# Optimization experiments

Measured on AMD Instinct MI355X. Metric: run time of the kernel, lower is better.

The kernel has to match this reference:

```python
import jax, jax.numpy as jnp
import numpy as np

B, S, H, T, F, L = 32, 512, 1024, 100, 512, 5  # batch, seq, hidden, num_topics, topic_hidden, n_langs
EPS = 1e-5


def _layernorm(x, g, b):
    mu = jnp.mean(x, axis=-1, keepdims=True)
    var = jnp.mean((x - mu) ** 2, axis=-1, keepdims=True)
    return (x - mu) * jax.lax.rsqrt(var + EPS) * g + b


def setup_inputs() -> dict:
    key = jax.random.key(0)
    ks = jax.random.split(key, 16)
    sc = 0.02
    return {
        "sequence_output": jax.random.normal(ks[0], (B, S, H), dtype=jnp.float32),
        "attention_mask": jnp.ones((B, S), dtype=jnp.float32),
        "language_ids": jax.random.randint(ks[1], (B,), 0, L, dtype=jnp.int32),
        "lda_features": jax.random.uniform(ks[2], (B, T), dtype=jnp.float32),
        # per-language adapter params (stacked over L)
        "W1": jax.random.normal(ks[3], (L, H, H), dtype=jnp.float32) * sc,
        "b1": jnp.zeros((L, H), dtype=jnp.float32),
        "g1": jnp.ones((L, H), dtype=jnp.float32),
        "beta1": jnp.zeros((L, H), dtype=jnp.float32),
        "W2": jax.random.normal(ks[4], (L, H, H), dtype=jnp.float32) * sc,
        "b2": jnp.zeros((L, H), dtype=jnp.float32),
        # topic fusion params
        "Wf": jax.random.normal(ks[5], (H + T, F), dtype=jnp.float32) * sc,
        "bf": jnp.zeros((F,), dtype=jnp.float32),
        "gf": jnp.ones((F,), dtype=jnp.float32),
        "betaf": jnp.zeros((F,), dtype=jnp.float32),
    }


def reference(sequence_output, attention_mask, language_ids, lda_features,
              W1, b1, g1, beta1, W2, b2, Wf, bf, gf, betaf):
    # Apply every language adapter to the full batch, then mask-accumulate
    # (faithful to the original anti-pattern).
    adapted = jnp.zeros_like(sequence_output)
    for lang in range(L):
        h = jnp.einsum("bsh,he->bse", sequence_output, W1[lang]) + b1[lang]
        h = jax.nn.relu(_layernorm(h, g1[lang], beta1[lang]))
        h = jnp.einsum("bsh,he->bse", h, W2[lang]) + b2[lang]
        lang_mask = (language_ids == lang).astype(sequence_output.dtype)[:, None, None]
        adapted = adapted + lang_mask * h
    # masked mean pool over sequence
    masked = adapted * attention_mask[:, :, None]
    pooled = masked.sum(axis=1) / attention_mask.sum(axis=1)[:, None]  # [B, H]
    combined = jnp.concatenate([pooled, lda_features], axis=-1)        # [B, H+T]
    fused = _layernorm(combined @ Wf + bf, gf, betaf)
    return jax.nn.relu(fused)  # dropout is identity in eval
```

## Files before the change

### kernel.cpp

```cpp
#include <hip/hip_runtime.h>
#include <hip/hip_bf16.h>
#include <stdint.h>

#define Bq 32
#define Sq 512
#define Hq 1024
#define Tq 100
#define Fq 512
#define Lq 5
#define EPSq 1e-5f

typedef float fx4 __attribute__((ext_vector_type(4)));
typedef __bf16 bfx8 __attribute__((ext_vector_type(8)));
typedef unsigned short u16x8 __attribute__((ext_vector_type(8)));

static __device__ __forceinline__ unsigned short f2bf(float f) {
  unsigned int u = __builtin_bit_cast(unsigned int, f);
  return (unsigned short)((u + 0x7fffu + ((u >> 16) & 1u)) >> 16);
}
static __device__ __forceinline__ float bf2f(unsigned short s) {
  return __builtin_bit_cast(float, ((unsigned int)s) << 16);
}
static __device__ __forceinline__ void gl_lds16(const void* g, void* l) {
  __builtin_amdgcn_global_load_lds(
      (const __attribute__((address_space(1))) unsigned int*)(uintptr_t)g,
      (__attribute__((address_space(3))) unsigned int*)(uintptr_t)l,
      16, 0, 0);
}

__global__ void k_prep(const float* __restrict__ seq, unsigned short* __restrict__ seqbf,
                       const float* __restrict__ w1, unsigned short* __restrict__ w1t) {
  int blk = blockIdx.x;
  int tid = threadIdx.x;
  if (blk < 8192) {
    int i = blk * 256 + tid;
    const float4* p = (const float4*)seq + (size_t)i * 2;
    float4 a = p[0], b = p[1];
    u16x8 o;
    o[0] = f2bf(a.x); o[1] = f2bf(a.y); o[2] = f2bf(a.z); o[3] = f2bf(a.w);
    o[4] = f2bf(b.x); o[5] = f2bf(b.y); o[6] = f2bf(b.z); o[7] = f2bf(b.w);
    *((u16x8*)seqbf + i) = o;
  } else {
    __shared__ float t[32][33];
    int bb = blk - 8192;
    int l = bb >> 10; int rem = bb & 1023; int tr = rem >> 5; int tc = rem & 31;
    const float* src = w1 + (size_t)l * Hq * Hq;
    unsigned short* dst = w1t + (size_t)l * Hq * Hq;
    int tx = tid & 31, ty = tid >> 5;
#pragma unroll
    for (int p = 0; p < 4; p++)
      t[ty + 8 * p][tx] = src[(size_t)(tr * 32 + ty + 8 * p) * Hq + tc * 32 + tx];
    __syncthreads();
#pragma unroll
    for (int p = 0; p < 4; p++)
      dst[(size_t)(tc * 32 + ty + 8 * p) * Hq + tr * 32 + tx] = f2bf(t[tx][ty + 8 * p]);
  }
}

__global__ __launch_bounds__(512, 2) void k_gemm1(const unsigned short* __restrict__ seqbf,
                                                  const unsigned short* __restrict__ w1t,
                                                  const float* __restrict__ b1,
                                                  const int* __restrict__ lid,
                                                  unsigned short* __restrict__ h1bf) {
  __shared__ short sA[4][256 * 32];
  __shared__ short sB[4][256 * 32];
  int bid = blockIdx.x;
  int g = bid & 63; int tn = bid >> 6;
  int b = g >> 1; int tm = g & 1;
  int lang = lid[b];
  const unsigned short* Ab = seqbf + (size_t)b * Sq * Hq + (size_t)tm * 256 * Hq;
  const unsigned short* Bb = w1t + (size_t)lang * Hq * Hq + (size_t)tn * 256 * Hq;

  int tid = threadIdx.x;
  int lane = tid & 63; int wid = tid >> 6;
  int wr = wid >> 2, wc = wid & 3;
  int fr = lane & 15;
  int q = lane >> 4;
  int key = ((fr >> 1) & 7) << 4;

  const unsigned short* gA[2]; const unsigned short* gB[2]; int dstOff[2];
#pragma unroll
  for (int j = 0; j < 2; j++) {
    int p = (tid + j * 512) * 16;
    int l = p ^ ((p >> 3) & 0x70);
    int R = l >> 6, qa = (l >> 4) & 3;
    gA[j] = Ab + (size_t)R * Hq + qa * 8;
    gB[j] = Bb + (size_t)R * Hq + qa * 8;
    dstOff[j] = p;
  }

  int aOff[8], bOff[4];
#pragma unroll
  for (int m = 0; m < 8; m++)
    aOff[m] = ((wr * 128 + m * 16 + fr) * 64 + q * 16) ^ key;
#pragma unroll
  for (int n = 0; n < 4; n++)
    bOff[n] = ((wc * 64 + n * 16 + fr) * 64 + q * 16) ^ key;

  fx4 acc[8][4];
#pragma unroll
  for (int m = 0; m < 8; m++)
#pragma unroll
    for (int n = 0; n < 4; n++) acc[m][n] = (fx4){0.f, 0.f, 0.f, 0.f};

#pragma unroll
  for (int s = 0; s < 3; s++) {
#pragma unroll
    for (int j = 0; j < 2; j++) {
      gl_lds16(gA[j] + s * 32, (char*)sA[s] + dstOff[j]);
      gl_lds16(gB[j] + s * 32, (char*)sB[s] + dstOff[j]);
    }
  }

  for (int hs = 0; hs < 32; hs++) {
    int cur = hs & 3;
    if (hs < 30)
      asm volatile("s_waitcnt vmcnt(8) lgkmcnt(0)\n\ts_barrier" ::: "memory");
    else if (hs == 30)
      asm volatile("s_waitcnt vmcnt(4) lgkmcnt(0)\n\ts_barrier" ::: "memory");
    else
      asm volatile("s_waitcnt vmcnt(0) lgkmcnt(0)\n\ts_barrier" ::: "memory");
    if (hs <= 28) {
      int slot = (hs + 3) & 3;
      int ko = (hs + 3) * 32;
#pragma unroll
      for (int j = 0; j < 2; j++) {
        gl_lds16(gA[j] + ko, (char*)sA[slot] + dstOff[j]);
        gl_lds16(gB[j] + ko, (char*)sB[slot] + dstOff[j]);
      }
    }
    const char* cA = (const char*)sA[cur];
    const char* cB = (const char*)sB[cur];
    bfx8 bf[4], af[8];
#pragma unroll
    for (int n = 0; n < 4; n++) bf[n] = *(const bfx8*)(cB + bOff[n]);
#pragma unroll
    for (int m = 0; m < 8; m++) af[m] = *(const bfx8*)(cA + aOff[m]);
    __builtin_amdgcn_s_setprio(1);
#pragma unroll
    for (int m = 0; m < 8; m++)
#pragma unroll
      for (int n = 0; n < 4; n++)
        acc[m][n] = __builtin_amdgcn_mfma_f32_16x16x32_bf16(af[m], bf[n], acc[m][n], 0, 0, 0);
    __builtin_amdgcn_s_setprio(0);
  }

  unsigned short* Cb = h1bf + (size_t)b * Sq * Hq;
  float bv[4];
#pragma unroll
  for (int n = 0; n < 4; n++)
    bv[n] = b1[lang * Hq + tn * 256 + wc * 64 + n * 16 + fr];
  int r0 = q * 4;
#pragma unroll
  for (int m = 0; m < 8; m++) {
#pragma unroll
    for (int n = 0; n < 4; n++) {
      int col = tn * 256 + wc * 64 + n * 16 + fr;
#pragma unroll
      for (int r = 0; r < 4; r++) {
        int row = tm * 256 + wr * 128 + m * 16 + r0 + r;
        Cb[(size_t)row * Hq + col] = f2bf(acc[m][n][r] + bv[n]);
      }
    }
  }
}

__global__ __launch_bounds__(256) void k_ln_pool(const unsigned short* __restrict__ h1bf,
                                                 const float* __restrict__ g1,
                                                 const float* __restrict__ be1,
                                                 const float* __restrict__ mask,
                                                 const int* __restrict__ lid,
                                                 float* __restrict__ partial) {
  __shared__ float sacc[4][1024];
  int blk = blockIdx.x; int b = blk >> 3; int ch = blk & 7;
  int tid = threadIdx.x; int lane = tid & 63; int w = tid >> 6;
  int lang = lid[b];
  int e0 = lane * 8;
  int e1 = 512 + lane * 8;

  const float4* gp = (const float4*)(g1 + (size_t)lang * Hq);
  const float4* bp = (const float4*)(be1 + (size_t)lang * Hq);
  float4 ga0 = gp[lane * 2], ga1 = gp[lane * 2 + 1];
  float4 gb0 = gp[128 + lane * 2], gb1 = gp[129 + lane * 2];
  float4 ba0 = bp[lane * 2], ba1 = bp[lane * 2 + 1];
  float4 bb0 = bp[128 + lane * 2], bb1 = bp[129 + lane * 2];
  float gA[8] = {ga0.x, ga0.y, ga0.z, ga0.w, ga1.x, ga1.y, ga1.z, ga1.w};
  float gB[8] = {gb0.x, gb0.y, gb0.z, gb0.w, gb1.x, gb1.y, gb1.z, gb1.w};
  float bA[8] = {ba0.x, ba0.y, ba0.z, ba0.w, ba1.x, ba1.y, ba1.z, ba1.w};
  float bB[8] = {bb0.x, bb0.y, bb0.z, bb0.w, bb1.x, bb1.y, bb1.z, bb1.w};

  float acc0[8] = {0, 0, 0, 0, 0, 0, 0, 0}, acc1[8] = {0, 0, 0, 0, 0, 0, 0, 0};

  for (int i = 0; i < 16; i++) {
    int s = ch * 64 + w * 16 + i;
    const unsigned short* rowp = h1bf + ((size_t)b * Sq + s) * Hq;
    u16x8 va = *(const u16x8*)(rowp + e0);
    u16x8 vb = *(const u16x8*)(rowp + e1);
    float xa[8], xb[8];
    float sum = 0.f, sq = 0.f;
#pragma unroll
    for (int j = 0; j < 8; j++) {
      xa[j] = bf2f(va[j]); sum += xa[j]; sq += xa[j] * xa[j];
      xb[j] = bf2f(vb[j]); sum += xb[j]; sq += xb[j] * xb[j];
    }
#pragma unroll
    for (int off = 1; off < 64; off <<= 1) {
      sum += __shfl_xor(sum, off, 64);
      sq += __shfl_xor(sq, off, 64);
    }
    float mu = sum * (1.f / Hq);
    float var = sq * (1.f / Hq) - mu * mu;
    float rstd = rsqrtf(var + EPSq);
    float mw = mask[b * Sq + s];
#pragma unroll
    for (int j = 0; j < 8; j++) {
      float y0 = fmaxf((xa[j] - mu) * rstd * gA[j] + bA[j], 0.f);
      float y1 = fmaxf((xb[j] - mu) * rstd * gB[j] + bB[j], 0.f);
      acc0[j] += mw * y0;
      acc1[j] += mw * y1;
    }
  }
#pragma unroll
  for (int j = 0; j < 8; j++) {
    sacc[w][e0 + j] = acc0[j];
    sacc[w][e1 + j] = acc1[j];
  }
  __syncthreads();
  int e = tid * 4;
#pragma unroll
  for (int j = 0; j < 4; j++)
    partial[(size_t)blk * Hq + e + j] =
        sacc[0][e + j] + sacc[1][e + j] + sacc[2][e + j] + sacc[3][e + j];
}

__global__ void k_reduce_pool(const float* __restrict__ partial, const float* __restrict__ mask,
                              float* __restrict__ pooled) {
  __shared__ float wsum[4];
  int b = blockIdx.x; int tid = threadIdx.x;
  float mv = mask[b * Sq + tid] + mask[b * Sq + 256 + tid];
#pragma unroll
  for (int off = 1; off < 64; off <<= 1) mv += __shfl_xor(mv, off, 64);
  if ((tid & 63) == 0) wsum[tid >> 6] = mv;
  __syncthreads();
  float inv = 1.0f / (wsum[0] + wsum[1] + wsum[2] + wsum[3]);
  int e = tid * 4;
#pragma unroll
  for (int j = 0; j < 4; j++) {
    float s = 0.f;
#pragma unroll
    for (int c = 0; c < 8; c++) s += partial[((size_t)b * 8 + c) * Hq + e + j];
    pooled[b * Hq + e + j] = s * inv;
  }
}

__global__ __launch_bounds__(256) void k_gemm2p(const float* __restrict__ pooled,
                                                const float* __restrict__ w2,
                                                const int* __restrict__ lid,
                                                float* __restrict__ g2part) {
  __shared__ float pl[256];
  int blk = blockIdx.x;
  int b = blk >> 3; int ch = (blk >> 2) & 1; int ks = blk & 3;
  int tid = threadIdx.x;
  int lang = lid[b];
  pl[tid] = pooled[b * Hq + ks * 256 + tid];
  __syncthreads();
  int col = ch * 512 + tid * 2;
  const float* W = w2 + (size_t)lang * Hq * Hq + (size_t)ks * 256 * Hq + col;
  float a0 = 0.f, a1 = 0.f;
  for (int e0 = 0; e0 < 256; e0 += 8) {
    float2 w[8];
#pragma unroll
    for (int j = 0; j < 8; j++) w[j] = *(const float2*)(W + (size_t)(e0 + j) * Hq);
#pragma unroll
    for (int j = 0; j < 8; j++) { float c = pl[e0 + j]; a0 += c * w[j].x; a1 += c * w[j].y; }
  }
  float2* dst = (float2*)(g2part + ((size_t)(b * 4 + ks) * Hq) + col);
  *dst = make_float2(a0, a1);
}

__global__ __launch_bounds__(256) void k_gemm2red(const float* __restrict__ g2part,
                                                  const float* __restrict__ b2,
                                                  const int* __restrict__ lid,
                                                  float* __restrict__ pooledf) {
  int b = blockIdx.x; int tid = threadIdx.x;
  int lang = lid[b];
  int col = tid * 4;
  float4 acc = *(const float4*)(b2 + (size_t)lang * Hq + col);
#pragma unroll
  for (int ks = 0; ks < 4; ks++) {
    float4 p = *(const float4*)(g2part + ((size_t)(b * 4 + ks) * Hq) + col);
    acc.x += p.x; acc.y += p.y; acc.z += p.z; acc.w += p.w;
  }
  *(float4*)(pooledf + (size_t)b * Hq + col) = acc;
}

__global__ __launch_bounds__(256) void k_fpart(const float* __restrict__ pooledf,
                                               const float* __restrict__ lda,
                                               const float* __restrict__ wf,
                                               float* __restrict__ fpart) {
  __shared__ float sc[128];
  int blk = blockIdx.x;
  int b = blk / 9, ks = blk % 9;
  int tid = threadIdx.x;
  int klen = (ks < 8) ? 128 : 100;
  int kbase = (ks < 8) ? ks * 128 : Hq;
  if (tid < klen) sc[tid] = (ks < 8) ? pooledf[b * Hq + kbase + tid] : lda[b * Tq + tid];
  __syncthreads();
  const float* W = wf + (size_t)kbase * Fq + tid * 2;
  float a0 = 0.f, a1 = 0.f;
  int k0 = 0;
  for (; k0 + 8 <= klen; k0 += 8) {
    float2 w[8];
#pragma unroll
    for (int j = 0; j < 8; j++) w[j] = *(const float2*)(W + (size_t)(k0 + j) * Fq);
#pragma unroll
    for (int j = 0; j < 8; j++) { float c = sc[k0 + j]; a0 += c * w[j].x; a1 += c * w[j].y; }
  }
  for (; k0 < klen; k0++) {
    float2 w = *(const float2*)(W + (size_t)k0 * Fq);
    float c = sc[k0];
    a0 += c * w.x; a1 += c * w.y;
  }
  float2* dst = (float2*)(fpart + (size_t)blk * Fq + tid * 2);
  *dst = make_float2(a0, a1);
}

__global__ __launch_bounds__(512) void k_final2(const float* __restrict__ fpart,
                                                const float* __restrict__ bff,
                                                const float* __restrict__ gf,
                                                const float* __restrict__ betaf,
                                                float* __restrict__ out) {
  __shared__ float rsum[8], rsq[8];
  int b = blockIdx.x; int tid = threadIdx.x;
  float acc = bff[tid];
#pragma unroll
  for (int ks = 0; ks < 9; ks++) acc += fpart[((size_t)b * 9 + ks) * Fq + tid];
  float s = acc, q = acc * acc;
#pragma unroll
  for (int off = 1; off < 64; off <<= 1) {
    s += __shfl_xor(s, off, 64);
    q += __shfl_xor(q, off, 64);
  }
  int w = tid >> 6, lane = tid & 63;
  if (lane == 0) { rsum[w] = s; rsq[w] = q; }
  __syncthreads();
  float S = 0.f, Q = 0.f;
#pragma unroll
  for (int i = 0; i < 8; i++) { S += rsum[i]; Q += rsq[i]; }
  float mu = S * (1.f / Fq);
  float var = Q * (1.f / Fq) - mu * mu;
  float y = (acc - mu) * rsqrtf(var + EPSq) * gf[tid] + betaf[tid];
  y = fmaxf(y, 0.f);
  out[b * Fq + tid] = y;
}

extern "C" void kernel_launch(void* const* d_in, const int* in_sizes, int n_in,
                              void* d_out, int out_size, void* d_ws, size_t ws_size,
                              hipStream_t stream) {
  const float* seq = (const float*)d_in[0];
  const float* mask = (const float*)d_in[1];
  const int* lid = (const int*)d_in[2];
  const float* lda = (const float*)d_in[3];
  const float* W1 = (const float*)d_in[4];
  const float* b1 = (const float*)d_in[5];
  const float* g1 = (const float*)d_in[6];
  const float* be1 = (const float*)d_in[7];
  const float* W2 = (const float*)d_in[8];
  const float* b2 = (const float*)d_in[9];
  const float* Wf = (const float*)d_in[10];
  const float* bff = (const float*)d_in[11];
  const float* gf = (const float*)d_in[12];
  const float* betaf = (const float*)d_in[13];
  float* out = (float*)d_out;

  char* ws = (char*)d_ws;
  unsigned short* seqbf = (unsigned short*)(ws);
  unsigned short* w1t = (unsigned short*)(ws + 33554432);
  unsigned short* h1bf = (unsigned short*)(ws + 44040192);
  float* partial = (float*)(ws + 77594624);
  float* pooled = (float*)(ws + 78643200);
  float* pooledf = (float*)(ws + 78774272);
  float* g2part = (float*)(ws + 78905344);
  float* fpart = (float*)(ws + 79429632);

  k_prep<<<13312, 256, 0, stream>>>(seq, seqbf, W1, w1t);
  k_gemm1<<<256, 512, 0, stream>>>(seqbf, w1t, b1, lid, h1bf);
  k_ln_pool<<<256, 256, 0, stream>>>(h1bf, g1, be1, mask, lid, partial);
  k_reduce_pool<<<32, 256, 0, stream>>>(partial, mask, pooled);
  k_gemm2p<<<256, 256, 0, stream>>>(pooled, W2, lid, g2part);
  k_gemm2red<<<32, 256, 0, stream>>>(g2part, b2, lid, pooledf);
  k_fpart<<<288, 256, 0, stream>>>(pooledf, lda, Wf, fpart);
  k_final2<<<32, 512, 0, stream>>>(fpart, bff, gf, betaf, out);
}
```

Measured before the change: 101.6 us.

## Fuse fp32-to-bf16 activation conversion into GEMM1 and merge small reduction kernels

Removes the separate sequence conversion pass: GEMM1 now loads fp32 activations into registers, converts to bf16 and writes swizzled LDS tiles, while B still uses direct global-to-LDS loads. The pooled reduction and bias-add reductions are folded into the downstream GEMV kernels, eliminating two launches and intermediate buffers. This trades a large extra memory pass for register pressure and VALU conversion work inside the GEMM main loop, with reworked wait counts.

```diff
diff --git a/kernel.cpp b/kernel.cpp
--- a/kernel.cpp
+++ b/kernel.cpp
@@ -21,6 +21,12 @@
 static __device__ __forceinline__ float bf2f(unsigned short s) {
   return __builtin_bit_cast(float, ((unsigned int)s) << 16);
 }
+static __device__ __forceinline__ u16x8 cvt8(float4 x0, float4 x1) {
+  u16x8 r;
+  r[0] = f2bf(x0.x); r[1] = f2bf(x0.y); r[2] = f2bf(x0.z); r[3] = f2bf(x0.w);
+  r[4] = f2bf(x1.x); r[5] = f2bf(x1.y); r[6] = f2bf(x1.z); r[7] = f2bf(x1.w);
+  return r;
+}
 static __device__ __forceinline__ void gl_lds16(const void* g, void* l) {
   __builtin_amdgcn_global_load_lds(
       (const __attribute__((address_space(1))) unsigned int*)(uintptr_t)g,
@@ -28,36 +34,24 @@
       16, 0, 0);
 }
 
-__global__ void k_prep(const float* __restrict__ seq, unsigned short* __restrict__ seqbf,
-                       const float* __restrict__ w1, unsigned short* __restrict__ w1t) {
+__global__ void k_prep(const float* __restrict__ w1, unsigned short* __restrict__ w1t) {
+  __shared__ float t[32][33];
   int blk = blockIdx.x;
+  int l = blk >> 10; int rem = blk & 1023; int tr = rem >> 5; int tc = rem & 31;
+  const float* src = w1 + (size_t)l * Hq * Hq;
+  unsigned short* dst = w1t + (size_t)l * Hq * Hq;
   int tid = threadIdx.x;
-  if (blk < 8192) {
-    int i = blk * 256 + tid;
-    const float4* p = (const float4*)seq + (size_t)i * 2;
-    float4 a = p[0], b = p[1];
-    u16x8 o;
-    o[0] = f2bf(a.x); o[1] = f2bf(a.y); o[2] = f2bf(a.z); o[3] = f2bf(a.w);
-    o[4] = f2bf(b.x); o[5] = f2bf(b.y); o[6] = f2bf(b.z); o[7] = f2bf(b.w);
-    *((u16x8*)seqbf + i) = o;
-  } else {
-    __shared__ float t[32][33];
-    int bb = blk - 8192;
-    int l = bb >> 10; int rem = bb & 1023; int tr = rem >> 5; int tc = rem & 31;
-    const float* src = w1 + (size_t)l * Hq * Hq;
-    unsigned short* dst = w1t + (size_t)l * Hq * Hq;
-    int tx = tid & 31, ty = tid >> 5;
-#pragma unroll
-    for (int p = 0; p < 4; p++)
-      t[ty + 8 * p][tx] = src[(size_t)(tr * 32 + ty + 8 * p) * Hq + tc * 32 + tx];
-    __syncthreads();
-#pragma unroll
-    for (int p = 0; p < 4; p++)
-      dst[(size_t)(tc * 32 + ty + 8 * p) * Hq + tr * 32 + tx] = f2bf(t[tx][ty + 8 * p]);
-  }
-}
-
-__global__ __launch_bounds__(512, 2) void k_gemm1(const unsigned short* __restrict__ seqbf,
+  int tx = tid & 31, ty = tid >> 5;
+#pragma unroll
+  for (int p = 0; p < 4; p++)
+    t[ty + 8 * p][tx] = src[(size_t)(tr * 32 + ty + 8 * p) * Hq + tc * 32 + tx];
+  __syncthreads();
+#pragma unroll
+  for (int p = 0; p < 4; p++)
+    dst[(size_t)(tc * 32 + ty + 8 * p) * Hq + tr * 32 + tx] = f2bf(t[tx][ty + 8 * p]);
+}
+
+__global__ __launch_bounds__(512, 2) void k_gemm1(const float* __restrict__ seq,
                                                   const unsigned short* __restrict__ w1t,
                                                   const float* __restrict__ b1,
                                                   const int* __restrict__ lid,
@@ -68,7 +62,7 @@
   int g = bid & 63; int tn = bid >> 6;
   int b = g >> 1; int tm = g & 1;
   int lang = lid[b];
-  const unsigned short* Ab = seqbf + (size_t)b * Sq * Hq + (size_t)tm * 256 * Hq;
+  const float* Abf = seq + (size_t)b * Sq * Hq + (size_t)tm * 256 * Hq;
   const unsigned short* Bb = w1t + (size_t)lang * Hq * Hq + (size_t)tn * 256 * Hq;
 
   int tid = threadIdx.x;
@@ -78,13 +72,21 @@
   int q = lane >> 4;
   int key = ((fr >> 1) & 7) << 4;
 
-  const unsigned short* gA[2]; const unsigned short* gB[2]; int dstOff[2];
+  const float* gAf0; const float* gAf1; int aW0, aW1;
+  {
+    int c0 = tid;        int R0 = c0 >> 2, q0 = c0 & 3; int y0 = R0 * 64 + q0 * 16;
+    int c1 = tid + 512;  int R1 = c1 >> 2, q1 = c1 & 3; int y1 = R1 * 64 + q1 * 16;
+    aW0 = y0 ^ ((y0 >> 3) & 0x70);
+    aW1 = y1 ^ ((y1 >> 3) & 0x70);
+    gAf0 = Abf + (size_t)R0 * Hq + q0 * 8;
+    gAf1 = Abf + (size_t)R1 * Hq + q1 * 8;
+  }
+  const unsigned short* gB[2]; int dstOff[2];
 #pragma unroll
   for (int j = 0; j < 2; j++) {
     int p = (tid + j * 512) * 16;
     int l = p ^ ((p >> 3) & 0x70);
     int R = l >> 6, qa = (l >> 4) & 3;
-    gA[j] = Ab + (size_t)R * Hq + qa * 8;
     gB[j] = Bb + (size_t)R * Hq + qa * 8;
     dstOff[j] = p;
   }
@@ -103,31 +105,43 @@
 #pragma unroll
     for (int n = 0; n < 4; n++) acc[m][n] = (fx4){0.f, 0.f, 0.f, 0.f};
 
+  float4 ra0a, ra0b, ra1a, ra1b;
+
+#pragma unroll
+  for (int t = 0; t < 2; t++) {
+    ra0a = *(const float4*)(gAf0 + t * 32); ra0b = *(const float4*)(gAf0 + t * 32 + 4);
+    ra1a = *(const float4*)(gAf1 + t * 32); ra1b = *(const float4*)(gAf1 + t * 32 + 4);
+    *(u16x8*)((char*)sA[t] + aW0) = cvt8(ra0a, ra0b);
+    *(u16x8*)((char*)sA[t] + aW1) = cvt8(ra1a, ra1b);
+  }
+  ra0a = *(const float4*)(gAf0 + 64); ra0b = *(const float4*)(gAf0 + 68);
+  ra1a = *(const float4*)(gAf1 + 64); ra1b = *(const float4*)(gAf1 + 68);
 #pragma unroll
   for (int s = 0; s < 3; s++) {
-#pragma unroll
-    for (int j = 0; j < 2; j++) {
-      gl_lds16(gA[j] + s * 32, (char*)sA[s] + dstOff[j]);
-      gl_lds16(gB[j] + s * 32, (char*)sB[s] + dstOff[j]);
-    }
+    gl_lds16(gB[0] + s * 32, (char*)sB[s] + dstOff[0]);
+    gl_lds16(gB[1] + s * 32, (char*)sB[s] + dstOff[1]);
   }
 
   for (int hs = 0; hs < 32; hs++) {
     int cur = hs & 3;
-    if (hs < 30)
-      asm volatile("s_waitcnt vmcnt(8) lgkmcnt(0)\n\ts_barrier" ::: "memory");
-    else if (hs == 30)
+    if (hs < 31)
       asm volatile("s_waitcnt vmcnt(4) lgkmcnt(0)\n\ts_barrier" ::: "memory");
     else
       asm volatile("s_waitcnt vmcnt(0) lgkmcnt(0)\n\ts_barrier" ::: "memory");
+    if (hs <= 29) {
+      int sa = (hs + 2) & 3;
+      *(u16x8*)((char*)sA[sa] + aW0) = cvt8(ra0a, ra0b);
+      *(u16x8*)((char*)sA[sa] + aW1) = cvt8(ra1a, ra1b);
+    }
     if (hs <= 28) {
-      int slot = (hs + 3) & 3;
       int ko = (hs + 3) * 32;
-#pragma unroll
-      for (int j = 0; j < 2; j++) {
-        gl_lds16(gA[j] + ko, (char*)sA[slot] + dstOff[j]);
-        gl_lds16(gB[j] + ko, (char*)sB[slot] + dstOff[j]);
-      }
+      ra0a = *(const float4*)(gAf0 + ko); ra0b = *(const float4*)(gAf0 + ko + 4);
+      ra1a = *(const float4*)(gAf1 + ko); ra1b = *(const float4*)(gAf1 + ko + 4);
+    }
+    if (hs <= 28) {
+      int ko = (hs + 3) * 32;
+      gl_lds16(gB[0] + ko, (char*)sB[(hs + 3) & 3] + dstOff[0]);
+      gl_lds16(gB[1] + ko, (char*)sB[(hs + 3) & 3] + dstOff[1]);
     }
     const char* cA = (const char*)sA[cur];
     const char* cB = (const char*)sB[cur];
@@ -233,36 +247,27 @@
         sacc[0][e + j] + sacc[1][e + j] + sacc[2][e + j] + sacc[3][e + j];
 }
 
-__global__ void k_reduce_pool(const float* __restrict__ partial, const float* __restrict__ mask,
-                              float* __restrict__ pooled) {
-  __shared__ float wsum[4];
-  int b = blockIdx.x; int tid = threadIdx.x;
-  float mv = mask[b * Sq + tid] + mask[b * Sq + 256 + tid];
-#pragma unroll
-  for (int off = 1; off < 64; off <<= 1) mv += __shfl_xor(mv, off, 64);
-  if ((tid & 63) == 0) wsum[tid >> 6] = mv;
-  __syncthreads();
-  float inv = 1.0f / (wsum[0] + wsum[1] + wsum[2] + wsum[3]);
-  int e = tid * 4;
-#pragma unroll
-  for (int j = 0; j < 4; j++) {
-    float s = 0.f;
-#pragma unroll
-    for (int c = 0; c < 8; c++) s += partial[((size_t)b * 8 + c) * Hq + e + j];
-    pooled[b * Hq + e + j] = s * inv;
-  }
-}
-
-__global__ __launch_bounds__(256) void k_gemm2p(const float* __restrict__ pooled,
+__global__ __launch_bounds__(256) void k_gemm2p(const float* __restrict__ partial,
+                                                const float* __restrict__ mask,
                                                 const float* __restrict__ w2,
                                                 const int* __restrict__ lid,
                                                 float* __restrict__ g2part) {
   __shared__ float pl[256];
+  __shared__ float wsum[4];
   int blk = blockIdx.x;
   int b = blk >> 3; int ch = (blk >> 2) & 1; int ks = blk & 3;
   int tid = threadIdx.x;
   int lang = lid[b];
-  pl[tid] = pooled[b * Hq + ks * 256 + tid];
+  float mv = mask[b * Sq + tid] + mask[b * Sq + 256 + tid];
+#pragma unroll
+  for (int off = 1; off < 64; off <<= 1) mv += __shfl_xor(mv, off, 64);
+  if ((tid & 63) == 0) wsum[tid >> 6] = mv;
+  __syncthreads();
+  float inv = 1.0f / (wsum[0] + wsum[1] + wsum[2] + wsum[3]);
+  float s = 0.f;
+#pragma unroll
+  for (int c = 0; c < 8; c++) s += partial[((size_t)(b * 8 + c)) * Hq + ks * 256 + tid];
+  pl[tid] = s * inv;
   __syncthreads();
   int col = ch * 512 + tid * 2;
   const float* W = w2 + (size_t)lang * Hq * Hq + (size_t)ks * 256 * Hq + col;
@@ -278,23 +283,9 @@
   *dst = make_float2(a0, a1);
 }
 
-__global__ __launch_bounds__(256) void k_gemm2red(const float* __restrict__ g2part,
-                                                  const float* __restrict__ b2,
-                                                  const int* __restrict__ lid,
-                                                  float* __restrict__ pooledf) {
-  int b = blockIdx.x; int tid = threadIdx.x;
-  int lang = lid[b];
-  int col = tid * 4;
-  float4 acc = *(const float4*)(b2 + (size_t)lang * Hq + col);
-#pragma unroll
-  for (int ks = 0; ks < 4; ks++) {
-    float4 p = *(const float4*)(g2part + ((size_t)(b * 4 + ks) * Hq) + col);
-    acc.x += p.x; acc.y += p.y; acc.z += p.z; acc.w += p.w;
-  }
-  *(float4*)(pooledf + (size_t)b * Hq + col) = acc;
-}
-
-__global__ __launch_bounds__(256) void k_fpart(const float* __restrict__ pooledf,
+__global__ __launch_bounds__(256) void k_fpart(const float* __restrict__ g2part,
+                                               const float* __restrict__ b2,
+                                               const int* __restrict__ lid,
                                                const float* __restrict__ lda,
                                                const float* __restrict__ wf,
                                                float* __restrict__ fpart) {
@@ -304,7 +295,17 @@
   int tid = threadIdx.x;
   int klen = (ks < 8) ? 128 : 100;
   int kbase = (ks < 8) ? ks * 128 : Hq;
-  if (tid < klen) sc[tid] = (ks < 8) ? pooledf[b * Hq + kbase + tid] : lda[b * Tq + tid];
+  if (ks < 8) {
+    if (tid < 128) {
+      int col = kbase + tid;
+      float v = b2[lid[b] * Hq + col];
+#pragma unroll
+      for (int c = 0; c < 4; c++) v += g2part[((size_t)(b * 4 + c)) * Hq + col];
+      sc[tid] = v;
+    }
+  } else if (tid < 100) {
+    sc[tid] = lda[b * Tq + tid];
+  }
   __syncthreads();
   const float* W = wf + (size_t)kbase * Fq + tid * 2;
   float a0 = 0.f, a1 = 0.f;
@@ -374,21 +375,16 @@
   float* out = (float*)d_out;
 
   char* ws = (char*)d_ws;
-  unsigned short* seqbf = (unsigned short*)(ws);
-  unsigned short* w1t = (unsigned short*)(ws + 33554432);
-  unsigned short* h1bf = (unsigned short*)(ws + 44040192);
-  float* partial = (float*)(ws + 77594624);
-  float* pooled = (float*)(ws + 78643200);
-  float* pooledf = (float*)(ws + 78774272);
-  float* g2part = (float*)(ws + 78905344);
-  float* fpart = (float*)(ws + 79429632);
-
-  k_prep<<<13312, 256, 0, stream>>>(seq, seqbf, W1, w1t);
-  k_gemm1<<<256, 512, 0, stream>>>(seqbf, w1t, b1, lid, h1bf);
+  unsigned short* w1t = (unsigned short*)(ws);
+  unsigned short* h1bf = (unsigned short*)(ws + 10485760);
+  float* partial = (float*)(ws + 44040192);
+  float* g2part = (float*)(ws + 45088768);
+  float* fpart = (float*)(ws + 45613056);
+
+  k_prep<<<5120, 256, 0, stream>>>(W1, w1t);
+  k_gemm1<<<256, 512, 0, stream>>>(seq, w1t, b1, lid, h1bf);
   k_ln_pool<<<256, 256, 0, stream>>>(h1bf, g1, be1, mask, lid, partial);
-  k_reduce_pool<<<32, 256, 0, stream>>>(partial, mask, pooled);
-  k_gemm2p<<<256, 256, 0, stream>>>(pooled, W2, lid, g2part);
-  k_gemm2red<<<32, 256, 0, stream>>>(g2part, b2, lid, pooledf);
-  k_fpart<<<288, 256, 0, stream>>>(pooledf, lda, Wf, fpart);
+  k_gemm2p<<<256, 256, 0, stream>>>(partial, mask, W2, lid, g2part);
+  k_fpart<<<288, 256, 0, stream>>>(g2part, b2, lid, lda, Wf, fpart);
   k_final2<<<32, 512, 0, stream>>>(fpart, bff, gf, betaf, out);
 }
```

Result: faster. 91.23 us (-10.2%).
